# Kernel tuning notes

Hardware: AMD Instinct MI355X
Metric: run time of the kernel (lower is better)

## Reference

```python
import jax, jax.numpy as jnp
import numpy as np

ALPHA, GAMMA = 0.25, 2.0
CLASS_W, COORD_W, MASK_W = 2.0, 5.0, 5.0
EPS = 1e-8


def point_sample(masks, coords):
    """Bilinear sample (grid_sample, align_corners=False, zero padding).
    masks: [R, H, W]; coords: [P, 2] as (x, y) in [0, 1]. Returns [R, P]."""
    H, W = masks.shape[-2:]
    gx = 2.0 * coords[:, 0] - 1.0
    gy = 2.0 * coords[:, 1] - 1.0
    x = ((gx + 1.0) * W - 1.0) * 0.5
    y = ((gy + 1.0) * H - 1.0) * 0.5
    x0 = jnp.floor(x)
    y0 = jnp.floor(y)
    wx1 = x - x0
    wy1 = y - y0
    wx0 = 1.0 - wx1
    wy0 = 1.0 - wy1
    x0i = x0.astype(jnp.int32)
    y0i = y0.astype(jnp.int32)
    x1i = x0i + 1
    y1i = y0i + 1

    def gather(ix, iy):
        valid = ((ix >= 0) & (ix < W) & (iy >= 0) & (iy < H)).astype(masks.dtype)
        ixc = jnp.clip(ix, 0, W - 1)
        iyc = jnp.clip(iy, 0, H - 1)
        return masks[:, iyc, ixc] * valid  # [R, P]

    return (gather(x0i, y0i) * (wx0 * wy0)
            + gather(x1i, y0i) * (wx1 * wy0)
            + gather(x0i, y1i) * (wx0 * wy1)
            + gather(x1i, y1i) * (wx1 * wy1))


def setup_inputs() -> dict:
    key = jax.random.key(0)
    k1, k2, k3, k4, k5, k6 = jax.random.split(key, 6)
    bs, Q, n_ctrl, Hm, Wm, T, P = 8, 300, 16, 128, 128, 160, 12544
    return {
        "pred_logits": jax.random.normal(k1, (bs, Q, 1), jnp.float32),
        "pred_ctrl_points": jax.random.uniform(k2, (bs, Q, n_ctrl, 2), jnp.float32),
        "pred_seg_mask": jax.random.normal(k3, (bs, Q, Hm, Wm), jnp.float32),
        "tgt_pts": jax.random.uniform(k4, (T, n_ctrl, 2), jnp.float32),
        "tgt_masks": jax.random.uniform(k5, (T, Hm, Wm), jnp.float32),
        "point_coords": jax.random.uniform(k6, (P, 2), jnp.float32),
        "lvl": 0,
    }


def reference(pred_logits, pred_ctrl_points, pred_seg_mask, tgt_pts, tgt_masks, point_coords, lvl):
    bs, Q = pred_logits.shape[:2]
    out_prob = jax.nn.sigmoid(pred_logits.reshape(bs * Q, -1))          # [N, 1]
    out_pts = pred_ctrl_points.reshape(bs * Q, -1)                      # [N, 2*n_ctrl]
    tgt_flat = tgt_pts.reshape(tgt_pts.shape[0], -1)                    # [T, 2*n_ctrl]

    cost_mask_dice = 0.0
    if lvl < 2:  # num_seg_layers
        out_masks = pred_seg_mask.reshape(bs * Q, *pred_seg_mask.shape[-2:])
        # nearest-interp of tgt_masks to out_masks size is identity (same size)
        t_pts_samp = point_sample(tgt_masks, point_coords)              # [T, P]
        o_pts_samp = point_sample(out_masks, point_coords)              # [N, P]
        s = jax.nn.sigmoid(o_pts_samp)                                  # dice_loss sigmoids inputs
        numerator = 2.0 * jnp.einsum('np,tp->nt', s, t_pts_samp)        # [N, T]
        denominator = s.sum(-1)[:, None] + t_pts_samp.sum(-1)[None, :]
        cost_mask_dice = 1.0 - (numerator + 1.0) / (denominator + 1.0)

    neg_cost = (1.0 - ALPHA) * out_prob ** GAMMA * (-jnp.log(1.0 - out_prob + EPS))
    pos_cost = ALPHA * (1.0 - out_prob) ** GAMMA * (-jnp.log(out_prob + EPS))
    cost_class = pos_cost - neg_cost                                    # [N, 1]

    cost_kpts = jnp.abs(out_pts[:, None, :] - tgt_flat[None, :, :]).sum(-1)  # L1 cdist [N, T]

    C = CLASS_W * cost_class + COORD_W * cost_kpts + MASK_W * cost_mask_dice
    return C.reshape(bs, Q, -1)
```

## Files before the change

kernel.cpp:

```cpp
#include <hip/hip_runtime.h>
#include <hip/hip_bf16.h>
#include <cstdint>

#define HW 128
#define MASK_ELEMS (HW * HW)
#define SBLK 1024
#define NBLK 256

typedef unsigned short ushort_t;
typedef __attribute__((ext_vector_type(4))) unsigned short ushort4_t;
typedef __attribute__((ext_vector_type(8))) short short8;
typedef __attribute__((ext_vector_type(4))) float f32x4;

__device__ __forceinline__ float asf(unsigned int u) {
    union { unsigned int i; float f; } c;
    c.i = u;
    return c.f;
}
__device__ __forceinline__ ushort_t f2bf(float f) {
    union { float f; unsigned int i; } c;
    c.f = f;
    unsigned int r = c.i + 0x7FFFu + ((c.i >> 16) & 1u);
    return (ushort_t)(r >> 16);
}

#define LDS_BARRIER()                                         \
    do {                                                      \
        asm volatile("s_waitcnt lgkmcnt(0)" ::: "memory");    \
        __builtin_amdgcn_s_barrier();                         \
    } while (0)

__global__ void kprep(const float* __restrict__ coords, int* __restrict__ idx,
                      uint2* __restrict__ wpk, int P) {
    int i = blockIdx.x * 256 + threadIdx.x;
    if (i >= P) return;
    float cx = coords[2 * i], cy = coords[2 * i + 1];
    float x = cx * (float)HW - 0.5f;
    float y = cy * (float)HW - 0.5f;
    float x0f = floorf(x), y0f = floorf(y);
    float wx1 = x - x0f, wy1 = y - y0f;
    float wx0 = 1.f - wx1, wy0 = 1.f - wy1;
    int x0 = (int)x0f, y0 = (int)y0f;

    float wxA = (x0 >= 0) ? wx0 : wx1;
    float wxB = (x0 >= 0 && x0 < HW - 1) ? wx1 : 0.f;
    float wyA = (y0 >= 0) ? wy0 : wy1;
    float wyB = (y0 >= 0 && y0 < HW - 1) ? wy1 : 0.f;
    int bx = max(x0, 0), by = max(y0, 0);
    if (bx > HW - 2) { bx = HW - 2; wxB = wxA; wxA = 0.f; }
    if (by > HW - 2) { by = HW - 2; wyB = wyA; wyA = 0.f; }

    idx[i] = by * HW + bx;
    wpk[i] = make_uint2((unsigned)f2bf(wxA * wyA) | ((unsigned)f2bf(wxB * wyA) << 16),
                        (unsigned)f2bf(wxA * wyB) | ((unsigned)f2bf(wxB * wyB) << 16));
}

__device__ __forceinline__ void load_mask_regs(const float* __restrict__ g, int tid,
                                               float4 rS[4], float rN[4]) {
    #pragma unroll
    for (int j = 0; j < 4; ++j) {
        int o = j * (SBLK * 4) + tid * 4;
        rS[j] = *(const float4*)(g + o);
        rN[j] = g[min(o + 4, MASK_ELEMS - 1)];
    }
}
__device__ __forceinline__ void pack_to_lds(unsigned* l, int tid, const float4 rS[4],
                                            const float rN[4]) {
    #pragma unroll
    for (int j = 0; j < 4; ++j) {
        int o = j * (SBLK * 4) + tid * 4;
        float4 v = rS[j];
        unsigned bx = (unsigned)f2bf(v.x), by = (unsigned)f2bf(v.y);
        unsigned bz = (unsigned)f2bf(v.z), bw = (unsigned)f2bf(v.w);
        unsigned bn = (unsigned)f2bf(rN[j]);
        uint4 e = make_uint4(bx | (by << 16), by | (bz << 16),
                             bz | (bw << 16), bw | (bn << 16));
        *(uint4*)&l[o] = e;
    }
}

__attribute__((amdgpu_waves_per_eu(4, 4)))
__global__ void __launch_bounds__(SBLK) ksamp_all(
        const float* __restrict__ pmask, const float* __restrict__ tmasks,
        const int* __restrict__ idx, const uint2* __restrict__ wpk,
        ushort_t* __restrict__ S, ushort_t* __restrict__ tsamp,
        float* __restrict__ ssum, float* __restrict__ tsum,
        const int* __restrict__ lvl, int N, int T, int P) {
    if (*lvl >= 2) return;
    __shared__ unsigned buf[2][MASK_ELEMS];
    __shared__ float wred[2][SBLK / 64];
    const int tid = threadIdx.x;
    const int NM = N + T;
    const int nq = P >> 2;

    int4 idr[4];
    uint4 war[4], wbr[4];
    #pragma unroll
    for (int it = 0; it < 4; ++it) {
        int q = it * SBLK + tid;
        if (q < nq) {
            idr[it] = ((const int4*)idx)[q];
            war[it] = ((const uint4*)wpk)[2 * q];
            wbr[it] = ((const uint4*)wpk)[2 * q + 1];
        } else {
            idr[it] = make_int4(0, 0, 0, 0);
            war[it] = make_uint4(0, 0, 0, 0);
            wbr[it] = make_uint4(0, 0, 0, 0);
        }
    }

    auto mptr = [&](int mi) -> const float* {
        return (mi < N) ? pmask + (size_t)mi * MASK_ELEMS
                        : tmasks + (size_t)(mi - N) * MASK_ELEMS;
    };

    const int b = blockIdx.x;
    const int rounds = (NM - b + NBLK - 1) / NBLK;
    if (rounds <= 0) return;

    float4 rS[4];
    float rN[4];
    load_mask_regs(mptr(b), tid, rS, rN);
    pack_to_lds(buf[0], tid, rS, rN);
    if (rounds > 1) load_mask_regs(mptr(b + NBLK), tid, rS, rN);
    LDS_BARRIER();

    int cur = 0;
    for (int k = 0; k < rounds; ++k) {
        if (k + 1 < rounds) {
            pack_to_lds(buf[cur ^ 1], tid, rS, rN);
            if (k + 2 < rounds)
                load_mask_regs(mptr(b + (k + 2) * NBLK), tid, rS, rN);
        }
        const unsigned* lm = buf[cur];
        const int mi = b + k * NBLK;
        const bool sig = (mi < N);
        ushort4_t* o4 = sig ? (ushort4_t*)(S + (size_t)mi * P)
                            : (ushort4_t*)(tsamp + (size_t)(mi - N) * P);
        float sum = 0.f;
        #pragma unroll
        for (int it = 0; it < 4; ++it) {
            int q = it * SBLK + tid;
            if (q < nq) {
                float v[4];
                int bi[4] = {idr[it].x, idr[it].y, idr[it].z, idr[it].w};
                unsigned wa[4] = {war[it].x, war[it].z, wbr[it].x, wbr[it].z};
                unsigned wb[4] = {war[it].y, war[it].w, wbr[it].y, wbr[it].w};
                #pragma unroll
                for (int p2 = 0; p2 < 4; ++p2) {
                    int bb = bi[p2];
                    unsigned r0 = lm[bb];
                    unsigned r1 = lm[bb + HW];
                    float vv = asf(wa[p2] << 16) * asf(r0 << 16)
                             + asf(wa[p2] & 0xffff0000u) * asf(r0 & 0xffff0000u)
                             + asf(wb[p2] << 16) * asf(r1 << 16)
                             + asf(wb[p2] & 0xffff0000u) * asf(r1 & 0xffff0000u);
                    if (sig) vv = __builtin_amdgcn_rcpf(1.f + __expf(-vv));
                    v[p2] = vv;
                }
                ushort4_t o = {f2bf(v[0]), f2bf(v[1]), f2bf(v[2]), f2bf(v[3])};
                o4[q] = o;
                sum += (v[0] + v[1]) + (v[2] + v[3]);
            }
        }
        #pragma unroll
        for (int m2 = 32; m2 > 0; m2 >>= 1) sum += __shfl_xor(sum, m2, 64);
        if ((tid & 63) == 0) wred[k & 1][tid >> 6] = sum;
        LDS_BARRIER();
        if (tid == 0) {
            float s = 0.f;
            #pragma unroll
            for (int w2 = 0; w2 < SBLK / 64; ++w2) s += wred[k & 1][w2];
            if (sig) ssum[mi] = s;
            else tsum[mi - N] = s;
        }
        cur ^= 1;
    }
}

#define LDF(Aarr, Barr, kof)                                                              \
    do {                                                                                  \
        _Pragma("unroll") for (int m_ = 0; m_ < 3; ++m_)                                  \
            Aarr[m_] = *(const short8*)(pa + (size_t)m_ * 16 * P + (kof));                \
        _Pragma("unroll") for (int j_ = 0; j_ < 5; ++j_)                                  \
            Barr[j_] = *(const short8*)(pb + (size_t)j_ * 16 * P + (kof));                \
    } while (0)

#define FMAS(Aarr, Barr)                                                                  \
    do {                                                                                  \
        _Pragma("unroll") for (int m_ = 0; m_ < 3; ++m_) {                                \
            _Pragma("unroll") for (int j_ = 0; j_ < 5; ++j_)                              \
                acc[m_][j_] = __builtin_amdgcn_mfma_f32_16x16x32_bf16(                    \
                    Aarr[m_], Barr[j_], acc[m_][j_], 0, 0, 0);                            \
        }                                                                                 \
    } while (0)

__global__ __launch_bounds__(256) void kgemm(const ushort_t* __restrict__ S,
                                             const ushort_t* __restrict__ Tm,
                                             float* __restrict__ Cpart,
                                             const int* __restrict__ lvl,
                                             int N, int T, int P, int nsteps) {
    if (*lvl >= 2) return;
    int tid = threadIdx.x;
    int wid = tid >> 6, lane = tid & 63;
    int wm = wid >> 1, wt = wid & 1;
    int r = lane & 15, g = lane >> 4;
    int n0 = blockIdx.x * 96 + wm * 48;
    int t0 = wt * 80;
    size_t k0 = (size_t)blockIdx.y * nsteps * 32 + g * 8;
    const ushort_t* pa = S + (size_t)(n0 + r) * P + k0;
    const ushort_t* pb = Tm + (size_t)(t0 + r) * P + k0;

    f32x4 acc[3][5];
    #pragma unroll
    for (int m2 = 0; m2 < 3; ++m2)
        #pragma unroll
        for (int j2 = 0; j2 < 5; ++j2) acc[m2][j2] = (f32x4){0.f, 0.f, 0.f, 0.f};

    short8 a0[3], b0[5], a1[3], b1[5];
    LDF(a0, b0, 0);
    int ks = 0;
    for (; ks + 2 < nsteps; ks += 2) {
        LDF(a1, b1, (ks + 1) * 32);
        FMAS(a0, b0);
        LDF(a0, b0, (ks + 2) * 32);
        FMAS(a1, b1);
    }
    LDF(a1, b1, (ks + 1) * 32);
    FMAS(a0, b0);
    FMAS(a1, b1);

    size_t cb = (size_t)blockIdx.y * N * T;
    #pragma unroll
    for (int m2 = 0; m2 < 3; ++m2)
        #pragma unroll
        for (int j2 = 0; j2 < 5; ++j2)
            #pragma unroll
            for (int q = 0; q < 4; ++q) {
                int row = n0 + m2 * 16 + g * 4 + q;
                int col = t0 + j2 * 16 + r;
                Cpart[cb + (size_t)row * T + col] = acc[m2][j2][q];
            }
}

__global__ void kfinal(const float* __restrict__ logits, const float* __restrict__ opts,
                       const float* __restrict__ tpts, const float* __restrict__ Cpart,
                       const float* __restrict__ ssum, const float* __restrict__ tsum,
                       const int* __restrict__ lvl, float* __restrict__ out,
                       int N, int T, int nks) {
    int idx = blockIdx.x * 256 + threadIdx.x;
    if (idx >= N * T) return;
    int n = idx / T, t = idx - n * T;

    float lg = logits[n];
    float p = 1.f / (1.f + __expf(-lg));
    float pos = 0.25f * (1.f - p) * (1.f - p) * (-logf(p + 1e-8f));
    float neg = 0.75f * p * p * (-logf(1.f - p + 1e-8f));
    float ccls = pos - neg;

    float kp = 0.f;
    const float4* a4 = (const float4*)(opts + (size_t)n * 32);
    const float4* b4 = (const float4*)(tpts + (size_t)t * 32);
    #pragma unroll
    for (int j = 0; j < 8; ++j) {
        float4 a = a4[j], b = b4[j];
        kp += fabsf(a.x - b.x) + fabsf(a.y - b.y) + fabsf(a.z - b.z) + fabsf(a.w - b.w);
    }

    float dice = 0.f;
    if (*lvl < 2) {
        float dot = 0.f;
        for (int ks = 0; ks < nks; ++ks) dot += Cpart[(size_t)ks * N * T + idx];
        dice = 1.f - (2.f * dot + 1.f) / (ssum[n] + tsum[t] + 1.f);
    }
    out[idx] = 2.f * ccls + 5.f * kp + 5.f * dice;
}

extern "C" void kernel_launch(void* const* d_in, const int* in_sizes, int n_in,
                              void* d_out, int out_size, void* d_ws, size_t ws_size,
                              hipStream_t stream) {
    const float* logits = (const float*)d_in[0];
    const float* cpts   = (const float*)d_in[1];
    const float* pmask  = (const float*)d_in[2];
    const float* tpts   = (const float*)d_in[3];
    const float* tmasks = (const float*)d_in[4];
    const float* coords = (const float*)d_in[5];
    const int*   lvl    = (const int*)d_in[6];
    float* out = (float*)d_out;

    int N = in_sizes[0];
    int T = in_sizes[3] / 32;
    int P = in_sizes[5] / 2;

    char* w = (char*)d_ws;
    auto alloc = [&](size_t bytes) {
        char* r = w;
        w += (bytes + 255) & ~(size_t)255;
        return r;
    };
    int*      idxb  = (int*)alloc((size_t)P * 4);
    uint2*    wpkb  = (uint2*)alloc((size_t)P * 8);
    ushort_t* tsamp = (ushort_t*)alloc((size_t)T * P * 2);
    ushort_t* S     = (ushort_t*)alloc((size_t)N * P * 2);
    float*    ssumb = (float*)alloc((size_t)N * 4);
    float*    tsumb = (float*)alloc((size_t)T * 4);
    size_t base_bytes = (size_t)(w - (char*)d_ws);

    int nks = 14;
    if (base_bytes + (size_t)nks * N * T * 4 > ws_size) nks = 7;
    int nsteps = (P / 32) / nks;
    float* Cpart = (float*)alloc((size_t)nks * N * T * 4);

    kprep<<<(P + 255) / 256, 256, 0, stream>>>(coords, idxb, wpkb, P);
    ksamp_all<<<NBLK, SBLK, 0, stream>>>(pmask, tmasks, idxb, wpkb, S, tsamp,
                                         ssumb, tsumb, lvl, N, T, P);
    kgemm<<<dim3(N / 96, nks), 256, 0, stream>>>(S, tsamp, Cpart, lvl, N, T, P, nsteps);
    kfinal<<<(N * T + 255) / 256, 256, 0, stream>>>(logits, cpts, tpts, Cpart, ssumb, tsumb,
                                                    lvl, out, N, T, nks);
}
```

Baseline: 119.3 us.

## Deepen mask prefetch to two rounds ahead and spread tail work across waves

```diff
diff --git a/kernel.cpp b/kernel.cpp
--- a/kernel.cpp
+++ b/kernel.cpp
@@ -29,6 +29,23 @@
         asm volatile("s_waitcnt lgkmcnt(0)" ::: "memory");    \
         __builtin_amdgcn_s_barrier();                         \
     } while (0)
+
+__device__ __forceinline__ int q_of(int it, int tid, int nq, bool& act) {
+    if (it < 3) {
+        int q = it * SBLK + tid;
+        act = (q < nq);
+        return q;
+    }
+    int rem = nq - 3 * SBLK;
+    if (rem == 64) {
+        int q = 3 * SBLK + (tid >> 4);
+        act = ((tid & 15) == 0);
+        return q;
+    }
+    int q = 3 * SBLK + tid;
+    act = (q < nq);
+    return q;
+}
 
 __global__ void kprep(const float* __restrict__ coords, int* __restrict__ idx,
                       uint2* __restrict__ wpk, int P) {
@@ -97,8 +114,9 @@
     uint4 war[4], wbr[4];
     #pragma unroll
     for (int it = 0; it < 4; ++it) {
-        int q = it * SBLK + tid;
-        if (q < nq) {
+        bool act;
+        int q = q_of(it, tid, nq, act);
+        if (act) {
             idr[it] = ((const int4*)idx)[q];
             war[it] = ((const uint4*)wpk)[2 * q];
             wbr[it] = ((const uint4*)wpk)[2 * q + 1];
@@ -118,19 +136,24 @@
     const int rounds = (NM - b + NBLK - 1) / NBLK;
     if (rounds <= 0) return;
 
-    float4 rS[4];
-    float rN[4];
-    load_mask_regs(mptr(b), tid, rS, rN);
-    pack_to_lds(buf[0], tid, rS, rN);
-    if (rounds > 1) load_mask_regs(mptr(b + NBLK), tid, rS, rN);
+    float4 sA[4], sB[4];
+    float nA[4], nB[4];
+    load_mask_regs(mptr(b), tid, sA, nA);
+    pack_to_lds(buf[0], tid, sA, nA);
+    if (rounds > 1) load_mask_regs(mptr(b + NBLK), tid, sB, nB);
+    if (rounds > 2) load_mask_regs(mptr(b + 2 * NBLK), tid, sA, nA);
     LDS_BARRIER();
 
     int cur = 0;
     for (int k = 0; k < rounds; ++k) {
         if (k + 1 < rounds) {
-            pack_to_lds(buf[cur ^ 1], tid, rS, rN);
-            if (k + 2 < rounds)
-                load_mask_regs(mptr(b + (k + 2) * NBLK), tid, rS, rN);
+            if (k & 1) {
+                pack_to_lds(buf[cur ^ 1], tid, sA, nA);
+                if (k + 3 < rounds) load_mask_regs(mptr(b + (k + 3) * NBLK), tid, sA, nA);
+            } else {
+                pack_to_lds(buf[cur ^ 1], tid, sB, nB);
+                if (k + 3 < rounds) load_mask_regs(mptr(b + (k + 3) * NBLK), tid, sB, nB);
+            }
         }
         const unsigned* lm = buf[cur];
         const int mi = b + k * NBLK;
@@ -140,8 +163,9 @@
         float sum = 0.f;
         #pragma unroll
         for (int it = 0; it < 4; ++it) {
-            int q = it * SBLK + tid;
-            if (q < nq) {
+            bool act;
+            int q = q_of(it, tid, nq, act);
+            if (act) {
                 float v[4];
                 int bi[4] = {idr[it].x, idr[it].y, idr[it].z, idr[it].w};
                 unsigned wa[4] = {war[it].x, war[it].z, wbr[it].x, wbr[it].z};
```

Result: slower. 189.6 us (+58.9%).

## Fuse point-prep into sampling kernel, shuffle neighbor values, trim register arrays

Applied to the files above, without the earlier changes.

```diff
diff --git a/kernel.cpp b/kernel.cpp
--- a/kernel.cpp
+++ b/kernel.cpp
@@ -23,6 +23,9 @@
     unsigned int r = c.i + 0x7FFFu + ((c.i >> 16) & 1u);
     return (ushort_t)(r >> 16);
 }
+__device__ __forceinline__ unsigned pack2(float a, float b) {
+    return (unsigned)f2bf(a) | ((unsigned)f2bf(b) << 16);
+}
 
 #define LDS_BARRIER()                                         \
     do {                                                      \
@@ -30,18 +33,14 @@
         __builtin_amdgcn_s_barrier();                         \
     } while (0)
 
-__global__ void kprep(const float* __restrict__ coords, int* __restrict__ idx,
-                      uint2* __restrict__ wpk, int P) {
-    int i = blockIdx.x * 256 + threadIdx.x;
-    if (i >= P) return;
-    float cx = coords[2 * i], cy = coords[2 * i + 1];
+struct PMeta { int b; unsigned u0, u1; };
+__device__ __forceinline__ PMeta prep_point(float cx, float cy) {
     float x = cx * (float)HW - 0.5f;
     float y = cy * (float)HW - 0.5f;
     float x0f = floorf(x), y0f = floorf(y);
     float wx1 = x - x0f, wy1 = y - y0f;
     float wx0 = 1.f - wx1, wy0 = 1.f - wy1;
     int x0 = (int)x0f, y0 = (int)y0f;
-
     float wxA = (x0 >= 0) ? wx0 : wx1;
     float wxB = (x0 >= 0 && x0 < HW - 1) ? wx1 : 0.f;
     float wyA = (y0 >= 0) ? wy0 : wy1;
@@ -49,65 +48,61 @@
     int bx = max(x0, 0), by = max(y0, 0);
     if (bx > HW - 2) { bx = HW - 2; wxB = wxA; wxA = 0.f; }
     if (by > HW - 2) { by = HW - 2; wyB = wyA; wyA = 0.f; }
-
-    idx[i] = by * HW + bx;
-    wpk[i] = make_uint2((unsigned)f2bf(wxA * wyA) | ((unsigned)f2bf(wxB * wyA) << 16),
-                        (unsigned)f2bf(wxA * wyB) | ((unsigned)f2bf(wxB * wyB) << 16));
-}
-
-__device__ __forceinline__ void load_mask_regs(const float* __restrict__ g, int tid,
-                                               float4 rS[4], float rN[4]) {
-    #pragma unroll
-    for (int j = 0; j < 4; ++j) {
-        int o = j * (SBLK * 4) + tid * 4;
-        rS[j] = *(const float4*)(g + o);
-        rN[j] = g[min(o + 4, MASK_ELEMS - 1)];
-    }
-}
-__device__ __forceinline__ void pack_to_lds(unsigned* l, int tid, const float4 rS[4],
-                                            const float rN[4]) {
-    #pragma unroll
-    for (int j = 0; j < 4; ++j) {
-        int o = j * (SBLK * 4) + tid * 4;
-        float4 v = rS[j];
-        unsigned bx = (unsigned)f2bf(v.x), by = (unsigned)f2bf(v.y);
-        unsigned bz = (unsigned)f2bf(v.z), bw = (unsigned)f2bf(v.w);
-        unsigned bn = (unsigned)f2bf(rN[j]);
-        uint4 e = make_uint4(bx | (by << 16), by | (bz << 16),
-                             bz | (bw << 16), bw | (bn << 16));
-        *(uint4*)&l[o] = e;
-    }
-}
-
-__attribute__((amdgpu_waves_per_eu(4, 4)))
-__global__ void __launch_bounds__(SBLK) ksamp_all(
+    PMeta m;
+    m.b = by * HW + bx;
+    m.u0 = pack2(wxA * wyA, wxB * wyA);
+    m.u1 = pack2(wxA * wyB, wxB * wyB);
+    return m;
+}
+
+__global__ __launch_bounds__(SBLK) void ksamp_all(
         const float* __restrict__ pmask, const float* __restrict__ tmasks,
-        const int* __restrict__ idx, const uint2* __restrict__ wpk,
+        const float* __restrict__ coords,
         ushort_t* __restrict__ S, ushort_t* __restrict__ tsamp,
         float* __restrict__ ssum, float* __restrict__ tsum,
         const int* __restrict__ lvl, int N, int T, int P) {
     if (*lvl >= 2) return;
     __shared__ unsigned buf[2][MASK_ELEMS];
     __shared__ float wred[2][SBLK / 64];
+    __shared__ int   tmi[256];
+    __shared__ uint4 tmw[256];
+    __shared__ int4  tmi4[64];
+    __shared__ uint4 tma[64], tmb[64];
     const int tid = threadIdx.x;
+    const int lane = tid & 63;
     const int NM = N + T;
     const int nq = P >> 2;
-
-    int4 idr[4];
-    uint4 war[4], wbr[4];
+    const int ntail = nq - 3 * SBLK;
+
+    int4 idr[3];
+    uint4 war[3], wbr[3];
     #pragma unroll
-    for (int it = 0; it < 4; ++it) {
+    for (int it = 0; it < 3; ++it) {
         int q = it * SBLK + tid;
         if (q < nq) {
-            idr[it] = ((const int4*)idx)[q];
-            war[it] = ((const uint4*)wpk)[2 * q];
-            wbr[it] = ((const uint4*)wpk)[2 * q + 1];
+            float4 ca = ((const float4*)coords)[2 * q];
+            float4 cb = ((const float4*)coords)[2 * q + 1];
+            PMeta m0 = prep_point(ca.x, ca.y), m1 = prep_point(ca.z, ca.w);
+            PMeta m2 = prep_point(cb.x, cb.y), m3 = prep_point(cb.z, cb.w);
+            idr[it] = make_int4(m0.b, m1.b, m2.b, m3.b);
+            war[it] = make_uint4(m0.u0, m0.u1, m1.u0, m1.u1);
+            wbr[it] = make_uint4(m2.u0, m2.u1, m3.u0, m3.u1);
         } else {
             idr[it] = make_int4(0, 0, 0, 0);
             war[it] = make_uint4(0, 0, 0, 0);
             wbr[it] = make_uint4(0, 0, 0, 0);
         }
     }
+    if (ntail > 0 && tid < ntail && tid < 64) {
+        int q = 3 * SBLK + tid;
+        float4 ca = ((const float4*)coords)[2 * q];
+        float4 cb = ((const float4*)coords)[2 * q + 1];
+        PMeta m0 = prep_point(ca.x, ca.y), m1 = prep_point(ca.z, ca.w);
+        PMeta m2 = prep_point(cb.x, cb.y), m3 = prep_point(cb.z, cb.w);
+        tmi4[tid] = make_int4(m0.b, m1.b, m2.b, m3.b);
+        tma[tid] = make_uint4(m0.u0, m0.u1, m1.u0, m1.u1);
+        tmb[tid] = make_uint4(m2.u0, m2.u1, m3.u0, m3.u1);
+    }
 
     auto mptr = [&](int mi) -> const float* {
         return (mi < N) ? pmask + (size_t)mi * MASK_ELEMS
@@ -119,18 +114,38 @@
     if (rounds <= 0) return;
 
     float4 rS[4];
-    float rN[4];
-    load_mask_regs(mptr(b), tid, rS, rN);
-    pack_to_lds(buf[0], tid, rS, rN);
-    if (rounds > 1) load_mask_regs(mptr(b + NBLK), tid, rS, rN);
+    float nxr[4];
+    auto load_mask = [&](const float* g) {
+        #pragma unroll
+        for (int j = 0; j < 4; ++j) {
+            int o = j * (SBLK * 4) + tid * 4;
+            rS[j] = *(const float4*)(g + o);
+            nxr[j] = (lane == 63) ? g[min(o + 4, MASK_ELEMS - 1)] : 0.f;
+        }
+    };
+    auto pack_mask = [&](unsigned* l) {
+        #pragma unroll
+        for (int j = 0; j < 4; ++j) {
+            int o = j * (SBLK * 4) + tid * 4;
+            float4 v = rS[j];
+            float nx = __shfl_down(v.x, 1);
+            if (lane == 63) nx = nxr[j];
+            uint4 e = make_uint4(pack2(v.x, v.y), pack2(v.y, v.z),
+                                 pack2(v.z, v.w), pack2(v.w, nx));
+            *(uint4*)&l[o] = e;
+        }
+    };
+
+    load_mask(mptr(b));
+    pack_mask(buf[0]);
+    if (rounds > 1) load_mask(mptr(b + NBLK));
     LDS_BARRIER();
 
     int cur = 0;
     for (int k = 0; k < rounds; ++k) {
         if (k + 1 < rounds) {
-            pack_to_lds(buf[cur ^ 1], tid, rS, rN);
-            if (k + 2 < rounds)
-                load_mask_regs(mptr(b + (k + 2) * NBLK), tid, rS, rN);
+            pack_mask(buf[cur ^ 1]);
+            if (k + 2 < rounds) load_mask(mptr(b + (k + 2) * NBLK));
         }
         const unsigned* lm = buf[cur];
         const int mi = b + k * NBLK;
@@ -138,34 +153,43 @@
         ushort4_t* o4 = sig ? (ushort4_t*)(S + (size_t)mi * P)
                             : (ushort4_t*)(tsamp + (size_t)(mi - N) * P);
         float sum = 0.f;
-        #pragma unroll
-        for (int it = 0; it < 4; ++it) {
+
+        auto do_quad = [&](int4 id, uint4 wa4, uint4 wb4, int q) {
+            float v[4];
+            int bi[4] = {id.x, id.y, id.z, id.w};
+            unsigned ua[4] = {wa4.x, wa4.z, wb4.x, wb4.z};
+            unsigned ub[4] = {wa4.y, wa4.w, wb4.y, wb4.w};
+            #pragma unroll
+            for (int p2 = 0; p2 < 4; ++p2) {
+                int bb = bi[p2];
+                unsigned r0 = lm[bb];
+                unsigned r1 = lm[bb + HW];
+                float vv = asf(ua[p2] << 16) * asf(r0 << 16)
+                         + asf(ua[p2] & 0xffff0000u) * asf(r0 & 0xffff0000u)
+                         + asf(ub[p2] << 16) * asf(r1 << 16)
+                         + asf(ub[p2] & 0xffff0000u) * asf(r1 & 0xffff0000u);
+                if (sig) vv = __builtin_amdgcn_rcpf(1.f + __expf(-vv));
+                v[p2] = vv;
+            }
+            ushort4_t o = {f2bf(v[0]), f2bf(v[1]), f2bf(v[2]), f2bf(v[3])};
+            o4[q] = o;
+            sum += (v[0] + v[1]) + (v[2] + v[3]);
+        };
+
+        #pragma unroll
+        for (int it = 0; it < 3; ++it) {
             int q = it * SBLK + tid;
-            if (q < nq) {
-                float v[4];
-                int bi[4] = {idr[it].x, idr[it].y, idr[it].z, idr[it].w};
-                unsigned wa[4] = {war[it].x, war[it].z, wbr[it].x, wbr[it].z};
-                unsigned wb[4] = {war[it].y, war[it].w, wbr[it].y, wbr[it].w};
-                #pragma unroll
-                for (int p2 = 0; p2 < 4; ++p2) {
-                    int bb = bi[p2];
-                    unsigned r0 = lm[bb];
-                    unsigned r1 = lm[bb + HW];
-                    float vv = asf(wa[p2] << 16) * asf(r0 << 16)
-                             + asf(wa[p2] & 0xffff0000u) * asf(r0 & 0xffff0000u)
-                             + asf(wb[p2] << 16) * asf(r1 << 16)
-                             + asf(wb[p2] & 0xffff0000u) * asf(r1 & 0xffff0000u);
-                    if (sig) vv = __builtin_amdgcn_rcpf(1.f + __expf(-vv));
-                    v[p2] = vv;
-                }
-                ushort4_t o = {f2bf(v[0]), f2bf(v[1]), f2bf(v[2]), f2bf(v[3])};
-                o4[q] = o;
-                sum += (v[0] + v[1]) + (v[2] + v[3]);
-            }
-        }
+            if (q < nq) do_quad(idr[it], war[it], wbr[it], q);
+        }
+        if (ntail > 0 && ntail <= 64) {
+            int tq = tid >> 4;
+            if (((tid & 15) == 0) && tq < ntail)
+                do_quad(tmi4[tq], tma[tq], tmb[tq], 3 * SBLK + tq);
+        }
+
         #pragma unroll
         for (int m2 = 32; m2 > 0; m2 >>= 1) sum += __shfl_xor(sum, m2, 64);
-        if ((tid & 63) == 0) wred[k & 1][tid >> 6] = sum;
+        if (lane == 0) wred[k & 1][tid >> 6] = sum;
         LDS_BARRIER();
         if (tid == 0) {
             float s = 0.f;
@@ -298,8 +322,6 @@
         w += (bytes + 255) & ~(size_t)255;
         return r;
     };
-    int*      idxb  = (int*)alloc((size_t)P * 4);
-    uint2*    wpkb  = (uint2*)alloc((size_t)P * 8);
     ushort_t* tsamp = (ushort_t*)alloc((size_t)T * P * 2);
     ushort_t* S     = (ushort_t*)alloc((size_t)N * P * 2);
     float*    ssumb = (float*)alloc((size_t)N * 4);
@@ -311,8 +333,7 @@
     int nsteps = (P / 32) / nks;
     float* Cpart = (float*)alloc((size_t)nks * N * T * 4);
 
-    kprep<<<(P + 255) / 256, 256, 0, stream>>>(coords, idxb, wpkb, P);
-    ksamp_all<<<NBLK, SBLK, 0, stream>>>(pmask, tmasks, idxb, wpkb, S, tsamp,
+    ksamp_all<<<NBLK, SBLK, 0, stream>>>(pmask, tmasks, coords, S, tsamp,
                                          ssumb, tsumb, lvl, N, T, P);
     kgemm<<<dim3(N / 96, nks), 256, 0, stream>>>(S, tsamp, Cpart, lvl, N, T, P, nsteps);
     kfinal<<<(N * T + 255) / 256, 256, 0, stream>>>(logits, cpts, tpts, Cpart, ssumb, tsumb,
```

After: 120.2 us. Within noise of the previous version (+0.8%).
